# Performance work log

Measured on AMD Instinct MI355X. Metric: run time of the kernel, lower is better.

## Reference

```python
import jax, jax.numpy as jnp
import numpy as np

BN_EPS = 1e-5


def gcn_conv(x, src, dst, n, W, b):
    # PyG GCNConv: h = x @ W; add self-loops; symmetric deg^{-1/2} norm; scatter-add; + bias
    h = x @ W
    sl = jnp.arange(n, dtype=src.dtype)
    src_f = jnp.concatenate([src, sl])
    dst_f = jnp.concatenate([dst, sl])
    deg = jax.ops.segment_sum(jnp.ones_like(dst_f, dtype=h.dtype), dst_f, num_segments=n)
    dis = jnp.where(deg > 0, jax.lax.rsqrt(jnp.maximum(deg, 1.0)), 0.0)
    norm = dis[src_f] * dis[dst_f]                       # [E+N]
    msg = h[src_f] * norm[:, None]                       # gather + scale
    out = jax.ops.segment_sum(msg, dst_f, num_segments=n)  # scatter-add
    return out + b


def batchnorm(x, g, b):
    # training-mode BatchNorm1d (batch statistics), deterministic
    mu = jnp.mean(x, axis=0)
    var = jnp.mean((x - mu) ** 2, axis=0)
    return g * (x - mu) * jax.lax.rsqrt(var + BN_EPS) + b


def setup_inputs() -> dict:
    key = jax.random.key(0)
    ks = jax.random.split(key, 12)
    N, E, F_IN, D, M, G = 40000, 640000, 128, 128, 256, 2000
    x = jax.random.normal(ks[0], (N, F_IN), dtype=jnp.float32)
    edge_index = jax.random.randint(ks[1], (2, E), 0, N, dtype=jnp.int64)
    batch = jnp.sort(jax.random.randint(ks[2], (N,), 0, G, dtype=jnp.int64))
    s = lambda fi: 1.0 / np.sqrt(fi)
    W1 = jax.random.normal(ks[3], (F_IN, D), dtype=jnp.float32) * s(F_IN)
    b1 = jnp.zeros((D,), jnp.float32)
    W2 = jax.random.normal(ks[4], (D, D), dtype=jnp.float32) * s(D)
    b2 = jnp.zeros((D,), jnp.float32)
    bn1_g = jnp.ones((D,), jnp.float32); bn1_b = jnp.zeros((D,), jnp.float32)
    bn2_g = jnp.ones((D,), jnp.float32); bn2_b = jnp.zeros((D,), jnp.float32)
    fc1_w = jax.random.normal(ks[5], (D, M), dtype=jnp.float32) * s(D)
    fc1_b = jnp.zeros((M,), jnp.float32)
    fc2_w = jax.random.normal(ks[6], (M, M), dtype=jnp.float32) * s(M)
    fc2_b = jnp.zeros((M,), jnp.float32)
    fc3_w = jax.random.normal(ks[7], (M, 1), dtype=jnp.float32) * s(M)
    fc3_b = jnp.zeros((1,), jnp.float32)
    return dict(x=x, edge_index=edge_index, batch=batch, num_graphs=G,
                W1=W1, b1=b1, W2=W2, b2=b2,
                bn1_g=bn1_g, bn1_b=bn1_b, bn2_g=bn2_g, bn2_b=bn2_b,
                fc1_w=fc1_w, fc1_b=fc1_b, fc2_w=fc2_w, fc2_b=fc2_b,
                fc3_w=fc3_w, fc3_b=fc3_b)


def reference(x, edge_index, batch, num_graphs, W1, b1, W2, b2,
              bn1_g, bn1_b, bn2_g, bn2_b,
              fc1_w, fc1_b, fc2_w, fc2_b, fc3_w, fc3_b):
    n = x.shape[0]
    src, dst = edge_index[0], edge_index[1]
    h = gcn_conv(x, src, dst, n, W1, b1)
    h = jax.nn.relu(batchnorm(h, bn1_g, bn1_b))
    h = gcn_conv(h, src, dst, n, W2, b2)
    h = jax.nn.relu(batchnorm(h, bn2_g, bn2_b))
    g = jax.ops.segment_sum(h, batch, num_segments=num_graphs)  # scatter_sum pooling [G, D]
    g = jax.nn.relu(g @ fc1_w + fc1_b)   # dropout is identity in eval
    g = jax.nn.relu(g @ fc2_w + fc2_b)
    return g @ fc3_w + fc3_b             # [G, 1]
```

## Files before the change

kernel.cpp:

```cpp
#include <hip/hip_runtime.h>
#include <hip/hip_fp16.h>

#define NN 40000
#define NE 640000
#define DF 128
#define NG 2000
#define NCH 157
#define FILLB 625
#define GT_BLKS 625
#define NCHUNK 16
#define ECH 40000
#define NOCT 8
#define QN 5120
#define NPAD (NOCT * QN)
#define NWIN 160
#define HISTB (NCHUNK * NOCT)
#define PREPB 144
#define NSLOT 16

typedef unsigned int u32;
typedef __attribute__((ext_vector_type(8))) short short8;
typedef __attribute__((ext_vector_type(4))) float floatx4;

__device__ inline float2 bf2_to_f2(u32 u) {
    return make_float2(__uint_as_float(u << 16), __uint_as_float(u & 0xffff0000u));
}
__device__ inline u32 f_to_bf(float f) {
    u32 u = __float_as_uint(f);
    return (u + 0x7fffu + ((u >> 16) & 1u)) >> 16;
}
__device__ inline u32 pack_bf2(float a, float b) {
    return f_to_bf(a) | (f_to_bf(b) << 16);
}
__device__ inline float bf_to_f(short s) {
    return __uint_as_float(((u32)(unsigned short)s) << 16);
}
__device__ inline float colw_to_f(int cw) {
    return __half2float(__ushort_as_half((unsigned short)((u32)cw >> 16)));
}

template<bool BF16IN, bool FUSE_BN>
__device__ __forceinline__ void gemm_core(const void* __restrict__ Xv, const unsigned short* __restrict__ wt,
                                          u32* __restrict__ outb, const float* __restrict__ slots,
                                          const float* __restrict__ gam, const float* __restrict__ bet,
                                          int bid, char* sbuf, float* sc, float* sh) {
    unsigned short* wlds = (unsigned short*)sbuf;
    unsigned short* clds = (unsigned short*)sbuf;
    int tid = threadIdx.x;
    int row0 = bid * 64;

    if (FUSE_BN) {
        if (tid < 128) {
            float s = 0.f, q = 0.f;
#pragma unroll
            for (int k = 0; k < NSLOT; k++) {
                s += slots[k * 256 + tid];
                q += slots[k * 256 + 128 + tid];
            }
            const float inv_n = 1.0f / (float)NN;
            float mu = s * inv_n;
            float va = fmaf(-mu, mu, q * inv_n);
            float a = gam[tid] * rsqrtf(va + 1e-5f);
            sc[tid] = a;
            sh[tid] = fmaf(-mu, a, bet[tid]);
        }
    }
    for (int i = tid; i < 2048; i += 256) {
        int c = i >> 4, s = i & 15;
        *(uint4*)&wlds[c * 128 + ((s ^ (c & 7)) << 3)] = ((const uint4*)wt)[i];
    }
    __syncthreads();

    int lane = tid & 63;
    int wave = tid >> 6;
    int qr = lane >> 4;
    int rl = lane & 15;

    int rA = row0 + wave * 16 + rl;
    floatx4 acc[8];
#pragma unroll
    for (int b = 0; b < 8; b++) acc[b] = (floatx4){0.f, 0.f, 0.f, 0.f};
#pragma unroll
    for (int kb = 0; kb < 4; kb++) {
        int k0 = kb * 32 + qr * 8;
        short8 a0;
        if (!BF16IN) {
            const float* p0 = (const float*)Xv + (size_t)rA * DF + k0;
            float4 u0 = *(const float4*)p0, u1 = *(const float4*)(p0 + 4);
            float fa[8] = {u0.x, u0.y, u0.z, u0.w, u1.x, u1.y, u1.z, u1.w};
#pragma unroll
            for (int j = 0; j < 8; j++) a0[j] = (short)f_to_bf(fa[j]);
        } else {
            a0 = *(const short8*)((const u32*)Xv + (size_t)rA * 64 + (k0 >> 1));
            if (FUSE_BN) {
#pragma unroll
                for (int j = 0; j < 8; j++) {
                    float f0 = fmaxf(fmaf(bf_to_f(a0[j]), sc[k0 + j], sh[k0 + j]), 0.f);
                    a0[j] = (short)f_to_bf(f0);
                }
            }
        }
#pragma unroll
        for (int ct = 0; ct < 8; ct++) {
            int rowB = ct * 16 + rl;
            short8 bfr = *(const short8*)&wlds[rowB * 128 + ((((kb << 2) + qr) ^ (rl & 7)) << 3)];
            acc[ct] = __builtin_amdgcn_mfma_f32_16x16x32_bf16(a0, bfr, acc[ct], 0, 0, 0);
        }
    }
    __syncthreads();
#pragma unroll
    for (int ct = 0; ct < 8; ct++)
#pragma unroll
        for (int r = 0; r < 4; r++) {
            int lr = wave * 16 + qr * 4 + r;
            int c = ct * 16 + rl;
            clds[lr * 128 + (((c >> 3) ^ (lr & 7)) << 3) + (c & 7)] = (unsigned short)f_to_bf(acc[ct][r]);
        }
    __syncthreads();
    for (int i = tid; i < 1024; i += 256) {
        int lr = i >> 4, s = i & 15;
        uint4 v = *(const uint4*)&clds[lr * 128 + ((s ^ (lr & 7)) << 3)];
        ((uint4*)(outb + (size_t)(row0 + lr) * 64))[s] = v;
    }
}

__global__ __launch_bounds__(256) void k_prephist(const float* __restrict__ W1, const float* __restrict__ W2,
                                                  unsigned short* __restrict__ wt1, unsigned short* __restrict__ wt2,
                                                  float* __restrict__ slots0,
                                                  const int* __restrict__ dst,
                                                  int* __restrict__ degT, int* __restrict__ rank,
                                                  int* __restrict__ wsum) {
    __shared__ __align__(16) char sbuf[20480];
    int bid = blockIdx.x, tid = threadIdx.x;
    if (bid < 16) {
        slots0[bid * 512 + tid] = 0.f;
        slots0[bid * 512 + 256 + tid] = 0.f;
        return;
    }
    if (bid < 80) {
        int i = (bid - 16) * 256 + tid;
        wt1[i] = (unsigned short)f_to_bf(W1[(i & 127) * 128 + (i >> 7)]);
        return;
    }
    if (bid < PREPB) {
        int i = (bid - 80) * 256 + tid;
        wt2[i] = (unsigned short)f_to_bf(W2[(i & 127) * 128 + (i >> 7)]);
        return;
    }
    int hb = bid - PREPB;
    int c = hb >> 3, oct = hb & 7;
    int nlo = oct * QN;
    int* hist = (int*)sbuf;
    for (int i = tid; i < QN; i += 256) hist[i] = 0;
    __syncthreads();
    int ebase = c * ECH;
    const int4* dst4 = (const int4*)(dst + ebase);
    for (int i4 = tid; i4 < 10000; i4 += 256) {
        int4 d4 = dst4[i4];
        int e = ebase + i4 * 4;
        int t0 = d4.x - nlo, t1 = d4.y - nlo, t2 = d4.z - nlo, t3 = d4.w - nlo;
        if ((u32)t0 < (u32)QN) rank[e]     = atomicAdd(&hist[t0], 1);
        if ((u32)t1 < (u32)QN) rank[e + 1] = atomicAdd(&hist[t1], 1);
        if ((u32)t2 < (u32)QN) rank[e + 2] = atomicAdd(&hist[t2], 1);
        if ((u32)t3 < (u32)QN) rank[e + 3] = atomicAdd(&hist[t3], 1);
    }
    __syncthreads();
    for (int i = tid; i < QN; i += 256) degT[(size_t)c * NPAD + nlo + i] = hist[i];
    int wv = tid >> 6, lane = tid & 63;
    for (int lw = wv; lw < 20; lw += 4) {
        int v = hist[lw * 256 + lane] + hist[lw * 256 + 64 + lane]
              + hist[lw * 256 + 128 + lane] + hist[lw * 256 + 192 + lane];
        for (int off = 32; off > 0; off >>= 1) v += __shfl_down(v, off);
        if (lane == 0) wsum[c * NWIN + oct * 20 + lw] = v;
    }
}

__global__ __launch_bounds__(256, 5) void k_scangemm(const int* __restrict__ degT, const int* __restrict__ wsum,
                                                     int* __restrict__ baseT,
                                                     int* __restrict__ row_ptr, float* __restrict__ dis,
                                                     const unsigned short* __restrict__ wt1,
                                                     const float* __restrict__ X, u32* __restrict__ outb) {
    __shared__ __align__(16) char sbuf[32768];
    int tid = threadIdx.x;
    int bid = blockIdx.x;
    if (bid < NCH) {
        int* red = (int*)sbuf;
        int* ls  = (int*)(sbuf + 1024);
        int wnd = bid;
        int part = 0;
        int wp = tid < NWIN ? tid : tid - NWIN;
        for (int idx = tid; idx < NCHUNK * NWIN; idx += 256) {
            if (wp < wnd) part += wsum[idx];
            wp += 96; if (wp >= NWIN) wp -= NWIN;
        }
        red[tid] = part;
        int n = wnd * 256 + tid;
        int run = 0;
#pragma unroll
        for (int c = 0; c < NCHUNK; c++) {
            int v = degT[(size_t)c * NPAD + n];
            baseT[(size_t)c * NPAD + n] = run;
            run += v;
        }
        int d = run;
        ls[tid] = d;
        __syncthreads();
#pragma unroll
        for (int off = 128; off > 0; off >>= 1) {
            if (tid < off) red[tid] += red[tid + off];
            __syncthreads();
        }
        int base = red[0];
#pragma unroll
        for (int off = 1; off < 256; off <<= 1) {
            int t = (tid >= off) ? ls[tid - off] : 0;
            __syncthreads();
            ls[tid] += t;
            __syncthreads();
        }
        if (n < NN) {
            int r = base + ls[tid] - d;
            row_ptr[n] = r;
            dis[n] = rsqrtf((float)(d + 1));
        }
        if (wnd == NCH - 1 && tid == 0) row_ptr[NN] = NE;
        return;
    }
    float* dummy = nullptr;
    gemm_core<false, false>(X, wt1, outb, nullptr, nullptr, nullptr,
                            bid - NCH, sbuf, dummy, dummy);
}

__global__ __launch_bounds__(256) void k_fill(const int* __restrict__ src, const int* __restrict__ dst,
                                              const int* __restrict__ rank, const int* __restrict__ row_ptr,
                                              const int* __restrict__ baseT,
                                              const float* __restrict__ dis, u32* __restrict__ col) {
    int i4 = blockIdx.x * 256 + threadIdx.x;
    int4 d4 = ((const int4*)dst)[i4];
    int4 s4 = ((const int4*)src)[i4];
    int4 r4 = ((const int4*)rank)[i4];
    int e = i4 * 4;
    int dd[4] = {d4.x, d4.y, d4.z, d4.w};
    int ss[4] = {s4.x, s4.y, s4.z, s4.w};
    int rr[4] = {r4.x, r4.y, r4.z, r4.w};
#pragma unroll
    for (int q = 0; q < 4; q++) {
        int c = (e + q) / ECH;
        u32 h = (u32)__half_as_ushort(__float2half(dis[ss[q]]));
        col[row_ptr[dd[q]] + baseT[(size_t)c * NPAD + dd[q]] + rr[q]] = (u32)ss[q] | (h << 16);
    }
}

__global__ __launch_bounds__(256, 4) void k_gemm2(const u32* __restrict__ Hb, const unsigned short* __restrict__ wt2,
                                                  u32* __restrict__ outb, const float* __restrict__ slots,
                                                  const float* __restrict__ gam, const float* __restrict__ bet) {
    __shared__ __align__(16) char sbuf[32768];
    __shared__ float sc[128], sh[128];
    gemm_core<true, true>(Hb, wt2, outb, slots, gam, bet, blockIdx.x, sbuf, sc, sh);
}

__global__ __launch_bounds__(256, 8) void k_gather(const u32* __restrict__ Hb, const int* __restrict__ row_ptr,
                                                   const u32* __restrict__ col, const float* __restrict__ dis,
                                                   const float* __restrict__ bias, u32* __restrict__ outb,
                                                   float* __restrict__ slots) {
    __shared__ float sred[4][128];
    __shared__ float qred[4][128];
    int t = threadIdx.x & 63;
    int wv = threadIdx.x >> 6;
    int node = blockIdx.x * 4 + wv;
    float di = dis[node];
    int lo = row_ptr[node], hi = row_ptr[node + 1];
    float2 acc;
    {
        float2 a = bf2_to_f2(Hb[(size_t)node * 64 + t]);
        acc = make_float2(a.x * di, a.y * di);
    }
    for (int base = lo; base < hi; base += 64) {
        int m = hi - base; if (m > 64) m = 64;
        int cw = 0;
        if (t < m) cw = (int)col[base + t];
        int ng = (m + 3) >> 2;
        int c[4]; u32 u[4];
#pragma unroll
        for (int q = 0; q < 4; q++) {
            int idx = q < m ? q : 0;
            c[q] = __shfl(cw, idx);
            u[q] = Hb[(size_t)(c[q] & 0xffff) * 64 + t];
        }
        for (int g = 1; g < ng; g++) {
            int c2[4]; u32 u2[4];
#pragma unroll
            for (int q = 0; q < 4; q++) {
                int ii = g * 4 + q;
                int idx = ii < m ? ii : 0;
                c2[q] = __shfl(cw, idx);
                u2[q] = Hb[(size_t)(c2[q] & 0xffff) * 64 + t];
            }
#pragma unroll
            for (int q = 0; q < 4; q++) {
                int ii = (g - 1) * 4 + q;
                float wq = ii < m ? colw_to_f(c[q]) : 0.f;
                float2 h = bf2_to_f2(u[q]);
                acc.x = fmaf(h.x, wq, acc.x);
                acc.y = fmaf(h.y, wq, acc.y);
            }
#pragma unroll
            for (int q = 0; q < 4; q++) { c[q] = c2[q]; u[q] = u2[q]; }
        }
#pragma unroll
        for (int q = 0; q < 4; q++) {
            int ii = (ng - 1) * 4 + q;
            float wq = ii < m ? colw_to_f(c[q]) : 0.f;
            float2 h = bf2_to_f2(u[q]);
            acc.x = fmaf(h.x, wq, acc.x);
            acc.y = fmaf(h.y, wq, acc.y);
        }
    }
    float2 b = ((const float2*)bias)[t];
    acc.x = fmaf(acc.x, di, b.x);
    acc.y = fmaf(acc.y, di, b.y);
    outb[(size_t)node * 64 + t] = pack_bf2(acc.x, acc.y);
    sred[wv][2 * t] = acc.x;     sred[wv][2 * t + 1] = acc.y;
    qred[wv][2 * t] = acc.x * acc.x; qred[wv][2 * t + 1] = acc.y * acc.y;
    __syncthreads();
    int tid = threadIdx.x;
    if (tid < 128) {
        float s = sred[0][tid] + sred[1][tid] + sred[2][tid] + sred[3][tid];
        float q = qred[0][tid] + qred[1][tid] + qred[2][tid] + qred[3][tid];
        int slot = blockIdx.x & (NSLOT - 1);
        atomicAdd(&slots[slot * 256 + tid], s);
        atomicAdd(&slots[slot * 256 + 128 + tid], q);
    }
}

__global__ __launch_bounds__(256) void k_poolfc(const u32* __restrict__ Hb, const int* __restrict__ batch,
                                                const float* __restrict__ slots,
                                                const float* __restrict__ gam, const float* __restrict__ bet,
                                                const float* __restrict__ fc1w, const float* __restrict__ fc1b,
                                                const float* __restrict__ fc2w, const float* __restrict__ fc2b,
                                                const float* __restrict__ fc3w, const float* __restrict__ fc3b,
                                                float* __restrict__ out) {
    __shared__ float sc[128], sh[128];
    __shared__ float pooled[4][128];
    __shared__ float g1[4][256];
    __shared__ float g2[4][256];
    __shared__ int bnds[5];
    int tid = threadIdx.x;
    int gbase = blockIdx.x * 4;
    if (tid < 128) {
        float s = 0.f, q = 0.f;
#pragma unroll
        for (int k = 0; k < NSLOT; k++) {
            s += slots[k * 256 + tid];
            q += slots[k * 256 + 128 + tid];
        }
        const float inv_n = 1.0f / (float)NN;
        float mu = s * inv_n;
        float va = fmaf(-mu, mu, q * inv_n);
        float a = gam[tid] * rsqrtf(va + 1e-5f);
        sc[tid] = a;
        sh[tid] = fmaf(-mu, a, bet[tid]);
    } else if (tid < 133) {
        int target = gbase + (tid - 128);
        int a = 0, b = NN;
        while (a < b) { int m = (a + b) >> 1; if (batch[m] < target) a = m + 1; else b = m; }
        bnds[tid - 128] = a;
    }
    __syncthreads();
    {
        int g = tid >> 6, p = tid & 63;
        int lo = bnds[g], hi = bnds[g + 1];
        float a0 = 0.f, a1 = 0.f;
        float sc0 = sc[2 * p], sh0 = sh[2 * p], sc1 = sc[2 * p + 1], sh1 = sh[2 * p + 1];
        for (int i = lo; i < hi; i++) {
            float2 v = bf2_to_f2(Hb[(size_t)i * 64 + p]);
            a0 += fmaxf(fmaf(v.x, sc0, sh0), 0.f);
            a1 += fmaxf(fmaf(v.y, sc1, sh1), 0.f);
        }
        pooled[g][2 * p] = a0;
        pooled[g][2 * p + 1] = a1;
    }
    __syncthreads();
    {
        float x0 = 0.f, x1 = 0.f, x2 = 0.f, x3 = 0.f;
        for (int k = 0; k < 128; k++) {
            float wv = fc1w[k * 256 + tid];
            x0 = fmaf(pooled[0][k], wv, x0);
            x1 = fmaf(pooled[1][k], wv, x1);
            x2 = fmaf(pooled[2][k], wv, x2);
            x3 = fmaf(pooled[3][k], wv, x3);
        }
        float bb = fc1b[tid];
        g1[0][tid] = fmaxf(x0 + bb, 0.f);
        g1[1][tid] = fmaxf(x1 + bb, 0.f);
        g1[2][tid] = fmaxf(x2 + bb, 0.f);
        g1[3][tid] = fmaxf(x3 + bb, 0.f);
    }
    __syncthreads();
    {
        float x0 = 0.f, x1 = 0.f, x2 = 0.f, x3 = 0.f;
        for (int k = 0; k < 256; k++) {
            float wv = fc2w[k * 256 + tid];
            x0 = fmaf(g1[0][k], wv, x0);
            x1 = fmaf(g1[1][k], wv, x1);
            x2 = fmaf(g1[2][k], wv, x2);
            x3 = fmaf(g1[3][k], wv, x3);
        }
        float bb = fc2b[tid];
        g2[0][tid] = fmaxf(x0 + bb, 0.f);
        g2[1][tid] = fmaxf(x1 + bb, 0.f);
        g2[2][tid] = fmaxf(x2 + bb, 0.f);
        g2[3][tid] = fmaxf(x3 + bb, 0.f);
    }
    __syncthreads();
    {
        int lane = tid & 63, wv = tid >> 6;
        float s = fmaf(g2[wv][lane], fc3w[lane],
                  fmaf(g2[wv][64 + lane], fc3w[64 + lane],
                  fmaf(g2[wv][128 + lane], fc3w[128 + lane],
                       g2[wv][192 + lane] * fc3w[192 + lane])));
        for (int off = 32; off > 0; off >>= 1) s += __shfl_down(s, off);
        if (lane == 0) out[gbase + wv] = s + fc3b[0];
    }
}

extern "C" void kernel_launch(void* const* d_in, const int* in_sizes, int n_in,
                              void* d_out, int out_size, void* d_ws, size_t ws_size,
                              hipStream_t stream) {
    const float* x    = (const float*)d_in[0];
    const int*   ei   = (const int*)d_in[1];
    const int*   batch= (const int*)d_in[2];
    const float* W1   = (const float*)d_in[4];
    const float* b1   = (const float*)d_in[5];
    const float* W2   = (const float*)d_in[6];
    const float* b2   = (const float*)d_in[7];
    const float* bn1g = (const float*)d_in[8];
    const float* bn1b = (const float*)d_in[9];
    const float* bn2g = (const float*)d_in[10];
    const float* bn2b = (const float*)d_in[11];
    const float* fc1w = (const float*)d_in[12];
    const float* fc1b = (const float*)d_in[13];
    const float* fc2w = (const float*)d_in[14];
    const float* fc2b = (const float*)d_in[15];
    const float* fc3w = (const float*)d_in[16];
    const float* fc3b = (const float*)d_in[17];
    const int* src = ei;
    const int* dst = ei + NE;
    float* outp = (float*)d_out;

    char* w = (char*)d_ws;
    size_t o = 0;
    auto alloc = [&](size_t bytes) -> char* {
        char* p = w + o;
        o = (o + bytes + 255) & ~(size_t)255;
        return p;
    };
    int*   degT    = (int*)alloc((size_t)NCHUNK * NPAD * 4);
    int*   baseT   = (int*)alloc((size_t)NCHUNK * NPAD * 4);
    int*   wsum    = (int*)alloc((size_t)NCHUNK * NWIN * 4);
    float* slots0  = (float*)alloc((size_t)2 * NSLOT * 256 * 4);
    int*   row_ptr = (int*)alloc((size_t)(NN + 1) * 4);
    int*   rank    = (int*)alloc((size_t)NE * 4);
    u32*   col     = (u32*)alloc((size_t)NE * 4);
    float* dis     = (float*)alloc((size_t)NN * 4);
    unsigned short* wt1 = (unsigned short*)alloc(128 * 128 * 2);
    unsigned short* wt2 = (unsigned short*)alloc(128 * 128 * 2);
    u32*   bufA    = (u32*)alloc((size_t)NN * 64 * 4);
    u32*   bufB    = (u32*)alloc((size_t)NN * 64 * 4);
    float* slotsA  = slots0;
    float* slotsB  = slots0 + NSLOT * 256;

    k_prephist<<<PREPB + HISTB, 256, 0, stream>>>(W1, W2, wt1, wt2, slots0,
                                                  dst, degT, rank, wsum);
    k_scangemm<<<NCH + GT_BLKS, 256, 0, stream>>>(degT, wsum, baseT, row_ptr, dis,
                                                  wt1, x, bufA);
    k_fill<<<FILLB, 256, 0, stream>>>(src, dst, rank, row_ptr, baseT, dis, col);
    k_gather<<<NN / 4, 256, 0, stream>>>(bufA, row_ptr, col, dis, b1, bufB, slotsA);
    k_gemm2<<<GT_BLKS, 256, 0, stream>>>(bufB, wt2, bufA, slotsA, bn1g, bn1b);
    k_gather<<<NN / 4, 256, 0, stream>>>(bufA, row_ptr, col, dis, b2, bufB, slotsB);
    k_poolfc<<<NG / 4, 256, 0, stream>>>(bufB, batch, slotsB, bn2g, bn2b,
                                         fc1w, fc1b, fc2w, fc2b, fc3w, fc3b, outp);
}
```

Before: 246.5 us.

## Split gather work into feature quarters with 16 nodes per block

```diff
diff --git a/kernel.cpp b/kernel.cpp
--- a/kernel.cpp
+++ b/kernel.cpp
@@ -8,6 +8,7 @@
 #define NCH 157
 #define FILLB 625
 #define GT_BLKS 625
+#define GATB 10000
 #define NCHUNK 16
 #define ECH 40000
 #define NOCT 8
@@ -15,8 +16,8 @@
 #define NPAD (NOCT * QN)
 #define NWIN 160
 #define HISTB (NCHUNK * NOCT)
-#define PREPB 144
-#define NSLOT 16
+#define PREPB 192
+#define NSLOT 64
 
 typedef unsigned int u32;
 typedef __attribute__((ext_vector_type(8))) short short8;
@@ -132,18 +133,18 @@
                                                   int* __restrict__ wsum) {
     __shared__ __align__(16) char sbuf[20480];
     int bid = blockIdx.x, tid = threadIdx.x;
-    if (bid < 16) {
+    if (bid < 64) {
         slots0[bid * 512 + tid] = 0.f;
         slots0[bid * 512 + 256 + tid] = 0.f;
         return;
     }
-    if (bid < 80) {
-        int i = (bid - 16) * 256 + tid;
+    if (bid < 128) {
+        int i = (bid - 64) * 256 + tid;
         wt1[i] = (unsigned short)f_to_bf(W1[(i & 127) * 128 + (i >> 7)]);
         return;
     }
     if (bid < PREPB) {
-        int i = (bid - 80) * 256 + tid;
+        int i = (bid - 128) * 256 + tid;
         wt2[i] = (unsigned short)f_to_bf(W2[(i & 127) * 128 + (i >> 7)]);
         return;
     }
@@ -263,42 +264,49 @@
                                                    const u32* __restrict__ col, const float* __restrict__ dis,
                                                    const float* __restrict__ bias, u32* __restrict__ outb,
                                                    float* __restrict__ slots) {
-    __shared__ float sred[4][128];
-    __shared__ float qred[4][128];
-    int t = threadIdx.x & 63;
-    int wv = threadIdx.x >> 6;
-    int node = blockIdx.x * 4 + wv;
+    __shared__ float sred[4][16][2];
+    __shared__ float qred[4][16][2];
+    int tid = threadIdx.x;
+    int lane = tid & 63;
+    int wv = tid >> 6;
+    int b = blockIdx.x;
+    int quarter = (b & 7) >> 1;
+    int ngrp = ((b >> 3) << 1) | (b & 1);
+    int g = lane >> 4, r = lane & 15;
+    int node = ngrp * 16 + wv * 4 + g;
+    int f = quarter * 16 + r;
     float di = dis[node];
     int lo = row_ptr[node], hi = row_ptr[node + 1];
     float2 acc;
     {
-        float2 a = bf2_to_f2(Hb[(size_t)node * 64 + t]);
+        float2 a = bf2_to_f2(Hb[(size_t)node * 64 + f]);
         acc = make_float2(a.x * di, a.y * di);
     }
-    for (int base = lo; base < hi; base += 64) {
-        int m = hi - base; if (m > 64) m = 64;
+    int lbase = lane & 48;
+    for (int base = lo; base < hi; base += 16) {
+        int m = hi - base; if (m > 16) m = 16;
         int cw = 0;
-        if (t < m) cw = (int)col[base + t];
+        if (r < m) cw = (int)col[base + r];
         int ng = (m + 3) >> 2;
         int c[4]; u32 u[4];
 #pragma unroll
         for (int q = 0; q < 4; q++) {
             int idx = q < m ? q : 0;
-            c[q] = __shfl(cw, idx);
-            u[q] = Hb[(size_t)(c[q] & 0xffff) * 64 + t];
-        }
-        for (int g = 1; g < ng; g++) {
+            c[q] = __shfl(cw, lbase + idx);
+            u[q] = Hb[(size_t)(c[q] & 0xffff) * 64 + f];
+        }
+        for (int gg = 1; gg < ng; gg++) {
             int c2[4]; u32 u2[4];
 #pragma unroll
             for (int q = 0; q < 4; q++) {
-                int ii = g * 4 + q;
+                int ii = gg * 4 + q;
                 int idx = ii < m ? ii : 0;
-                c2[q] = __shfl(cw, idx);
-                u2[q] = Hb[(size_t)(c2[q] & 0xffff) * 64 + t];
+                c2[q] = __shfl(cw, lbase + idx);
+                u2[q] = Hb[(size_t)(c2[q] & 0xffff) * 64 + f];
             }
 #pragma unroll
             for (int q = 0; q < 4; q++) {
-                int ii = (g - 1) * 4 + q;
+                int ii = (gg - 1) * 4 + q;
                 float wq = ii < m ? colw_to_f(c[q]) : 0.f;
                 float2 h = bf2_to_f2(u[q]);
                 acc.x = fmaf(h.x, wq, acc.x);
@@ -316,20 +324,28 @@
             acc.y = fmaf(h.y, wq, acc.y);
         }
     }
-    float2 b = ((const float2*)bias)[t];
-    acc.x = fmaf(acc.x, di, b.x);
-    acc.y = fmaf(acc.y, di, b.y);
-    outb[(size_t)node * 64 + t] = pack_bf2(acc.x, acc.y);
-    sred[wv][2 * t] = acc.x;     sred[wv][2 * t + 1] = acc.y;
-    qred[wv][2 * t] = acc.x * acc.x; qred[wv][2 * t + 1] = acc.y * acc.y;
-    __syncthreads();
-    int tid = threadIdx.x;
-    if (tid < 128) {
-        float s = sred[0][tid] + sred[1][tid] + sred[2][tid] + sred[3][tid];
-        float q = qred[0][tid] + qred[1][tid] + qred[2][tid] + qred[3][tid];
-        int slot = blockIdx.x & (NSLOT - 1);
-        atomicAdd(&slots[slot * 256 + tid], s);
-        atomicAdd(&slots[slot * 256 + 128 + tid], q);
+    float2 bb = ((const float2*)bias)[f];
+    acc.x = fmaf(acc.x, di, bb.x);
+    acc.y = fmaf(acc.y, di, bb.y);
+    outb[(size_t)node * 64 + f] = pack_bf2(acc.x, acc.y);
+    float sx = acc.x, sy = acc.y, qx = acc.x * acc.x, qy = acc.y * acc.y;
+    sx += __shfl_xor(sx, 16); sx += __shfl_xor(sx, 32);
+    sy += __shfl_xor(sy, 16); sy += __shfl_xor(sy, 32);
+    qx += __shfl_xor(qx, 16); qx += __shfl_xor(qx, 32);
+    qy += __shfl_xor(qy, 16); qy += __shfl_xor(qy, 32);
+    if (lane < 16) {
+        sred[wv][r][0] = sx; sred[wv][r][1] = sy;
+        qred[wv][r][0] = qx; qred[wv][r][1] = qy;
+    }
+    __syncthreads();
+    if (tid < 32) {
+        int rr = tid >> 1, side = tid & 1;
+        float s = sred[0][rr][side] + sred[1][rr][side] + sred[2][rr][side] + sred[3][rr][side];
+        float q = qred[0][rr][side] + qred[1][rr][side] + qred[2][rr][side] + qred[3][rr][side];
+        int colx = 2 * (quarter * 16 + rr) + side;
+        int slot = b & (NSLOT - 1);
+        atomicAdd(&slots[slot * 256 + colx], s);
+        atomicAdd(&slots[slot * 256 + 128 + colx], q);
     }
 }
 
@@ -475,9 +491,9 @@
     k_scangemm<<<NCH + GT_BLKS, 256, 0, stream>>>(degT, wsum, baseT, row_ptr, dis,
                                                   wt1, x, bufA);
     k_fill<<<FILLB, 256, 0, stream>>>(src, dst, rank, row_ptr, baseT, dis, col);
-    k_gather<<<NN / 4, 256, 0, stream>>>(bufA, row_ptr, col, dis, b1, bufB, slotsA);
+    k_gather<<<GATB, 256, 0, stream>>>(bufA, row_ptr, col, dis, b1, bufB, slotsA);
     k_gemm2<<<GT_BLKS, 256, 0, stream>>>(bufB, wt2, bufA, slotsA, bn1g, bn1b);
-    k_gather<<<NN / 4, 256, 0, stream>>>(bufA, row_ptr, col, dis, b2, bufB, slotsB);
+    k_gather<<<GATB, 256, 0, stream>>>(bufA, row_ptr, col, dis, b2, bufB, slotsB);
     k_poolfc<<<NG / 4, 256, 0, stream>>>(bufB, batch, slotsB, bn2g, bn2b,
                                          fc1w, fc1b, fc2w, fc2b, fc3w, fc3b, outp);
 }
```

Result: no change. 250.5 us (+1.6%).
